# Kernel tuning notes

Measured on AMD Instinct MI355X. Metric: run time of the kernel, lower is better.

## Reference

```python
import jax, jax.numpy as jnp
import numpy as np
import math

B, T, D, H, P, NPASS = 2, 2048, 1024, 16, 256, 3


def setup_inputs() -> dict:
    key = jax.random.key(0)
    ks = jax.random.split(key, 8)
    x = jax.random.normal(ks[0], (B, T, D), jnp.float32)
    scale_gamma = 1.0 + 0.1 * jax.random.normal(ks[1], (D,), jnp.float32)
    scale_beta = 0.1 * jax.random.normal(ks[2], (D,), jnp.float32)
    qkv_w = 0.02 * jax.random.normal(ks[3], (3 * D, D), jnp.float32)
    o_w = 0.02 * jax.random.normal(ks[4], (D, D), jnp.float32)
    norm1_w = jnp.ones((D,), jnp.float32)
    norm2_w = jnp.ones((D,), jnp.float32)
    angles = 0.1 * jax.random.normal(ks[5], (NPASS, P), jnp.float32)
    gate = jnp.ones((NPASS, D), jnp.float32)
    bias = jnp.zeros((NPASS, D), jnp.float32)
    # seeded random permutations matching torch.manual_seed(42+p*1000); torch.randperm
    pis, pjs = [], []
    for p in range(NPASS):
        rng = np.random.RandomState(42 + p * 1000)
        perm = rng.permutation(D)
        pis.append(perm[:P])
        pjs.append(perm[P:2 * P])
    pi = jnp.asarray(np.stack(pis), jnp.int32)
    pj = jnp.asarray(np.stack(pjs), jnp.int32)
    return dict(x=x, scale_gamma=scale_gamma, scale_beta=scale_beta, qkv_w=qkv_w,
                o_w=o_w, norm1_w=norm1_w, norm2_w=norm2_w, angles=angles,
                gate=gate, bias=bias, pi=pi, pj=pj)


def _rmsnorm(x, w):
    eps = jnp.finfo(x.dtype).eps
    return x * jax.lax.rsqrt(jnp.mean(x * x, axis=-1, keepdims=True) + eps) * w


def reference(x, scale_gamma, scale_beta, qkv_w, o_w, norm1_w, norm2_w,
              angles, gate, bias, pi, pj):
    Bs, Ts, Ds = x.shape
    hd = Ds // H
    # --- attention branch ---
    h = _rmsnorm(x, norm1_w) * scale_gamma + scale_beta
    qkv = (h @ qkv_w.T).reshape(Bs, Ts, 3, H, hd)
    qkv = jnp.moveaxis(qkv, 2, 0)            # [3, B, T, H, hd]
    q, k, v = (jnp.swapaxes(qkv[i], 1, 2) for i in range(3))  # [B, H, T, hd]
    scores = jnp.einsum('bhqd,bhkd->bhqk', q, k) / math.sqrt(hd)
    causal = jnp.tril(jnp.ones((Ts, Ts), bool))
    scores = jnp.where(causal, scores, -jnp.inf)
    attn = jax.nn.softmax(scores, axis=-1)
    out = jnp.einsum('bhqk,bhkd->bhqd', attn, v)
    out = jnp.swapaxes(out, 1, 2).reshape(Bs, Ts, Ds)
    x = x + out @ o_w.T
    # --- rotation pseudo-FFN branch ---
    h = _rmsnorm(x, norm2_w) * scale_gamma + scale_beta
    r = h
    for p in range(NPASS):
        cos_a = jnp.cos(angles[p])
        sin_a = jnp.sin(angles[p])
        hi = r[..., pi[p]]
        hj = r[..., pj[p]]
        r = r.at[..., pi[p]].set(hi * cos_a - hj * sin_a)
        r = r.at[..., pj[p]].set(hi * sin_a + hj * cos_a)
        r = jax.nn.silu(r * gate[p] + bias[p])
    return x + r - h
```

## Files before the change

kernel.cpp:

```cpp
#include <hip/hip_runtime.h>
#include <hip/hip_bf16.h>

#define B_ 2
#define T_ 2048
#define D_ 1024
#define H_ 16
#define HD_ 64
#define NP_ 3
#define P_ 256

#define SCALE2 0.18033688011112042f

typedef short bf16x8 __attribute__((ext_vector_type(8)));
typedef float f32x4 __attribute__((ext_vector_type(4)));

__device__ __forceinline__ float bf2f(__hip_bfloat16 v) { return __bfloat162float(v); }
__device__ __forceinline__ __hip_bfloat16 f2bf(float v) { return __float2bfloat16(v); }

__device__ __forceinline__ unsigned pack2bf(float a, float b) {
    union { __hip_bfloat16 h; unsigned short u; } ua, ub;
    ua.h = f2bf(a); ub.h = f2bf(b);
    return (unsigned)ua.u | ((unsigned)ub.u << 16);
}

#define GLOAD_LDS16(gp, lp) \
    __builtin_amdgcn_global_load_lds( \
        (const __attribute__((address_space(1))) void*)(gp), \
        (__attribute__((address_space(3))) void*)(lp), 16, 0, 0)

__global__ __launch_bounds__(256) void detect_kernel(
    const unsigned short* __restrict__ xs, int* __restrict__ flag)
{
    __shared__ int cnt;
    if (threadIdx.x == 0) cnt = 0;
    __syncthreads();
    int bad = 0;
    for (int i = threadIdx.x; i < 16384; i += 256) {
        int e = (xs[i] >> 7) & 0xFF;
        if (e >= 0xB8) bad++;
    }
    if (bad) atomicAdd(&cnt, bad);
    __syncthreads();
    if (threadIdx.x == 0) *flag = (cnt >= 8) ? 1 : 0;
}

__global__ __launch_bounds__(256) void cvt16_2_kernel(
    const void* __restrict__ a, const void* __restrict__ bsrc,
    __hip_bfloat16* __restrict__ da, __hip_bfloat16* __restrict__ db,
    int na, int ntot, const int* __restrict__ flag)
{
    int i = blockIdx.x * 256 + threadIdx.x;
    if (i >= ntot) return;
    int f = *flag;
    if (i < na)
        da[i] = f ? f2bf(((const float*)a)[i]) : ((const __hip_bfloat16*)a)[i];
    else {
        int k = i - na;
        db[k] = f ? f2bf(((const float*)bsrc)[k]) : ((const __hip_bfloat16*)bsrc)[k];
    }
}

__global__ __launch_bounds__(256) void cvt_small_kernel(
    const void* __restrict__ g,  const void* __restrict__ b,
    const void* __restrict__ n1, const void* __restrict__ n2,
    const void* __restrict__ ang, const void* __restrict__ gt,
    const void* __restrict__ bi,
    float* __restrict__ dst, const int* __restrict__ flag)
{
    int i = blockIdx.x * 256 + threadIdx.x;
    if (i >= 11008) return;
    const void* src; int off;
    if      (i < 1024) { src = g;   off = i; }
    else if (i < 2048) { src = b;   off = i - 1024; }
    else if (i < 3072) { src = n1;  off = i - 2048; }
    else if (i < 4096) { src = n2;  off = i - 3072; }
    else if (i < 4864) { src = ang; off = i - 4096; }
    else if (i < 7936) { src = gt;  off = i - 4864; }
    else               { src = bi;  off = i - 7936; }
    dst[i] = (*flag) ? ((const float*)src)[off]
                     : bf2f(((const __hip_bfloat16*)src)[off]);
}

__global__ __launch_bounds__(256) void rmsnorm1_kernel(
    const void* __restrict__ xraw,
    const float* __restrict__ gamma,
    const float* __restrict__ beta,
    const float* __restrict__ w,
    const int* __restrict__ flag,
    __hip_bfloat16* __restrict__ out,
    float* __restrict__ xcopy)
{
    int row = blockIdx.x;
    int t = threadIdx.x;
    int f = *flag;
    float eps = f ? 1.1920929e-7f : 0.0078125f;
    float v[4];
    if (f) {
        const float4 xv = ((const float4*)((const float*)xraw + (size_t)row * D_))[t];
        v[0] = xv.x; v[1] = xv.y; v[2] = xv.z; v[3] = xv.w;
    } else {
        const __hip_bfloat16* xr = (const __hip_bfloat16*)xraw + (size_t)row * D_;
#pragma unroll
        for (int c = 0; c < 4; c++) v[c] = bf2f(xr[t * 4 + c]);
    }
    float ss = 0.f;
#pragma unroll
    for (int c = 0; c < 4; c++) ss += v[c] * v[c];
#pragma unroll
    for (int m = 32; m; m >>= 1) ss += __shfl_xor(ss, m, 64);
    __shared__ float red[4];
    int wv = t >> 6;
    if ((t & 63) == 0) red[wv] = ss;
    __syncthreads();
    float scale = rsqrtf((red[0] + red[1] + red[2] + red[3]) * (1.0f / D_) + eps);
#pragma unroll
    for (int c = 0; c < 4; c++) {
        int e = t * 4 + c;
        size_t idx = (size_t)row * D_ + e;
        xcopy[idx] = v[c];
        out[idx] = f2bf(v[c] * scale * w[e] * gamma[e] + beta[e]);
    }
}

__global__ __launch_bounds__(256) void gemm_bt_bf16_kernel(
    const __hip_bfloat16* __restrict__ A,
    const __hip_bfloat16* __restrict__ Bm,
    __hip_bfloat16* __restrict__ C,
    int M, int N, int K, int nscale, float qscale)
{
    __shared__ __attribute__((aligned(16))) __hip_bfloat16 As[128 * 32];
    __shared__ __attribute__((aligned(16))) __hip_bfloat16 Bs[128 * 32];
    int tid = threadIdx.x;
    int bm = blockIdx.y, bn = blockIdx.x;
    int lane = tid & 63, wv = tid >> 6;
    int wm = wv >> 1, wn = wv & 1;
    int q = lane >> 4, mr = lane & 15;

    f32x4 acc[4][4] = {};

    for (int k0 = 0; k0 < K; k0 += 32) {
#pragma unroll
        for (int s = 0; s < 2; s++) {
            int e = (s * 256 + tid) * 8;
            int r = e >> 5, c = e & 31;
            GLOAD_LDS16(&A[(size_t)(bm * 128 + r) * K + k0 + c], &As[e]);
            GLOAD_LDS16(&Bm[(size_t)(bn * 128 + r) * K + k0 + c], &Bs[e]);
        }
        __syncthreads();
        bf16x8 af[4], bfr[4];
#pragma unroll
        for (int i = 0; i < 4; i++)
            af[i] = *(const bf16x8*)(&As[(wm * 64 + i * 16 + mr) * 32 + q * 8]);
#pragma unroll
        for (int j = 0; j < 4; j++)
            bfr[j] = *(const bf16x8*)(&Bs[(wn * 64 + j * 16 + mr) * 32 + q * 8]);
#pragma unroll
        for (int i = 0; i < 4; i++)
#pragma unroll
            for (int j = 0; j < 4; j++)
                acc[i][j] = __builtin_amdgcn_mfma_f32_16x16x32_bf16(af[i], bfr[j], acc[i][j], 0, 0, 0);
        __syncthreads();
    }

#pragma unroll
    for (int i = 0; i < 4; i++)
#pragma unroll
        for (int r = 0; r < 4; r++) {
            int m = bm * 128 + wm * 64 + i * 16 + q * 4 + r;
#pragma unroll
            for (int j = 0; j < 4; j++) {
                int n = bn * 128 + wn * 64 + j * 16 + mr;
                float vv = acc[i][j][r];
                if (n < nscale) vv *= qscale;
                C[(size_t)m * N + n] = f2bf(vv);
            }
        }
}

__global__ __launch_bounds__(256) void gemm_bt_resid_kernel(
    const __hip_bfloat16* __restrict__ A,
    const __hip_bfloat16* __restrict__ Bm,
    const float* __restrict__ resid,
    float* __restrict__ C,
    int M, int N, int K)
{
    __shared__ __attribute__((aligned(16))) __hip_bfloat16 As[128 * 32];
    __shared__ __attribute__((aligned(16))) __hip_bfloat16 Bs[128 * 32];
    int tid = threadIdx.x;
    int bm = blockIdx.y, bn = blockIdx.x;
    int lane = tid & 63, wv = tid >> 6;
    int wm = wv >> 1, wn = wv & 1;
    int q = lane >> 4, mr = lane & 15;

    f32x4 acc[4][4] = {};

    for (int k0 = 0; k0 < K; k0 += 32) {
#pragma unroll
        for (int s = 0; s < 2; s++) {
            int e = (s * 256 + tid) * 8;
            int r = e >> 5, c = e & 31;
            GLOAD_LDS16(&A[(size_t)(bm * 128 + r) * K + k0 + c], &As[e]);
            GLOAD_LDS16(&Bm[(size_t)(bn * 128 + r) * K + k0 + c], &Bs[e]);
        }
        __syncthreads();
        bf16x8 af[4], bfr[4];
#pragma unroll
        for (int i = 0; i < 4; i++)
            af[i] = *(const bf16x8*)(&As[(wm * 64 + i * 16 + mr) * 32 + q * 8]);
#pragma unroll
        for (int j = 0; j < 4; j++)
            bfr[j] = *(const bf16x8*)(&Bs[(wn * 64 + j * 16 + mr) * 32 + q * 8]);
#pragma unroll
        for (int i = 0; i < 4; i++)
#pragma unroll
            for (int j = 0; j < 4; j++)
                acc[i][j] = __builtin_amdgcn_mfma_f32_16x16x32_bf16(af[i], bfr[j], acc[i][j], 0, 0, 0);
        __syncthreads();
    }

#pragma unroll
    for (int i = 0; i < 4; i++)
#pragma unroll
        for (int r = 0; r < 4; r++) {
            int m = bm * 128 + wm * 64 + i * 16 + q * 4 + r;
#pragma unroll
            for (int j = 0; j < 4; j++) {
                int n = bn * 128 + wn * 64 + j * 16 + mr;
                size_t idx = (size_t)m * N + n;
                C[idx] = resid[idx] + acc[i][j][r];
            }
        }
}

__global__ __launch_bounds__(256, 4) void attn_kernel(
    const __hip_bfloat16* __restrict__ qkv,
    __hip_bfloat16* __restrict__ attn_out)
{
    __shared__ __attribute__((aligned(16))) __hip_bfloat16 Ks[2][64 * 64];
    __shared__ __attribute__((aligned(16))) __hip_bfloat16 Vts[2][64 * 64];
    __shared__ __attribute__((aligned(16))) unsigned int Pd[4 * 512];

    int z = blockIdx.x;
    int qt0 = 31 - z, qt1 = z;
    int bh = blockIdx.y;
    int b = bh >> 4, h = bh & 15;
    int tid = threadIdx.x, lane = tid & 63, wv = tid >> 6;
    int q = lane >> 4, mr = lane & 15;
    int m8 = mr & 7;

    const size_t rs3 = 3 * D_;
    const __hip_bfloat16* qp = qkv + (size_t)(b * T_) * rs3 + h * HD_;
    const __hip_bfloat16* kp = qp + D_;
    const __hip_bfloat16* vp = qp + 2 * D_;

    int sr = tid >> 2;
    int sc = (tid & 3) * 16;
    int lc0 = sc >> 3;
    int swk = sr & 7;
    int kk_ = (tid & 31) * 2;
    int dd = (tid >> 5) * 8;
    int vlc = kk_ >> 3, voff = kk_ & 7;

    bf16x8 aq0, aq1, aqn0, aqn1;
    {
        const __hip_bfloat16* qrow = qp + (size_t)(qt0 * 64 + wv * 16 + mr) * rs3;
        aq0 = *(const bf16x8*)(qrow + q * 8);
        aq1 = *(const bf16x8*)(qrow + 32 + q * 8);
    }

    bf16x8 kr0 = *(const bf16x8*)(kp + (size_t)sr * rs3 + sc);
    bf16x8 kr1 = *(const bf16x8*)(kp + (size_t)sr * rs3 + sc + 8);
    bf16x8 vr0 = *(const bf16x8*)(vp + (size_t)kk_ * rs3 + dd);
    bf16x8 vr1 = *(const bf16x8*)(vp + (size_t)(kk_ + 1) * rs3 + dd);
    *(bf16x8*)(&Ks[0][sr * 64 + ((lc0 ^ swk) * 8)]) = kr0;
    *(bf16x8*)(&Ks[0][sr * 64 + (((lc0 + 1) ^ swk) * 8)]) = kr1;
    {
        unsigned int* vd = (unsigned int*)&Vts[0][0];
#pragma unroll
        for (int i = 0; i < 8; i++) {
            unsigned int wd = ((unsigned int)(unsigned short)vr0[i]) |
                              (((unsigned int)(unsigned short)vr1[i]) << 16);
            vd[((dd + i) * 64 + ((vlc ^ i) * 8 + voff)) >> 1] = wd;
        }
    }
    __syncthreads();

    float m_run = -INFINITY, l_run = 0.f;
    f32x4 o_acc[4] = {};
    unsigned int* Pw = &Pd[wv * 512];
    int qloc = wv * 16 + mr;

    for (int s = 0; s <= 32; s++) {
        int seg1 = (s > qt0);
        int kt = seg1 ? (s - qt0 - 1) : s;
        int qt = seg1 ? qt1 : qt0;
        int buf = s & 1;

        if (s < 32) {
            int ktn = (s + 1 > qt0) ? (s - qt0) : (s + 1);
            kr0 = *(const bf16x8*)(kp + (size_t)(ktn * 64 + sr) * rs3 + sc);
            kr1 = *(const bf16x8*)(kp + (size_t)(ktn * 64 + sr) * rs3 + sc + 8);
            vr0 = *(const bf16x8*)(vp + (size_t)(ktn * 64 + kk_) * rs3 + dd);
            vr1 = *(const bf16x8*)(vp + (size_t)(ktn * 64 + kk_ + 1) * rs3 + dd);
        }
        if (s == qt0) {
            const __hip_bfloat16* qrow = qp + (size_t)(qt1 * 64 + wv * 16 + mr) * rs3;
            aqn0 = *(const bf16x8*)(qrow + q * 8);
            aqn1 = *(const bf16x8*)(qrow + 32 + q * 8);
        }

        f32x4 sv[4] = {};
        {
            const __hip_bfloat16* Kb = &Ks[buf][0];
#pragma unroll
            for (int jn = 0; jn < 4; jn++)
                sv[jn] = __builtin_amdgcn_mfma_f32_16x16x32_bf16(
                    *(const bf16x8*)(&Kb[(jn * 16 + mr) * 64 + ((q ^ m8) * 8)]),
                    aq0, sv[jn], 0, 0, 0);
#pragma unroll
            for (int jn = 0; jn < 4; jn++)
                sv[jn] = __builtin_amdgcn_mfma_f32_16x16x32_bf16(
                    *(const bf16x8*)(&Kb[(jn * 16 + mr) * 64 + (((4 + q) ^ m8) * 8)]),
                    aq1, sv[jn], 0, 0, 0);
        }

        if (kt == qt) {
#pragma unroll
            for (int jn = 0; jn < 4; jn++)
#pragma unroll
                for (int r = 0; r < 4; r++)
                    if (jn * 16 + q * 4 + r > qloc) sv[jn][r] = -1e30f;
        }

        float mx = fmaxf(fmaxf(sv[0][0], sv[0][1]), fmaxf(sv[0][2], sv[0][3]));
#pragma unroll
        for (int jn = 1; jn < 4; jn++)
            mx = fmaxf(mx, fmaxf(fmaxf(sv[jn][0], sv[jn][1]), fmaxf(sv[jn][2], sv[jn][3])));
        mx = fmaxf(mx, __shfl_xor(mx, 16, 64));
        mx = fmaxf(mx, __shfl_xor(mx, 32, 64));
        float mn = fmaxf(m_run, mx);
        float alpha = exp2f(m_run - mn);
        m_run = mn;
        float psum = 0.f;
#pragma unroll
        for (int jn = 0; jn < 4; jn++)
#pragma unroll
            for (int r = 0; r < 4; r++) {
                float p = exp2f(sv[jn][r] - mn);
                sv[jn][r] = p;
                psum += p;
            }
        psum += __shfl_xor(psum, 16, 64);
        psum += __shfl_xor(psum, 32, 64);
        l_run = l_run * alpha + psum;
#pragma unroll
        for (int dt = 0; dt < 4; dt++)
#pragma unroll
            for (int r = 0; r < 4; r++)
                o_acc[dt][r] *= alpha;

#pragma unroll
        for (int jn = 0; jn < 4; jn++) {
            uint2 val;
            val.x = pack2bf(sv[jn][0], sv[jn][1]);
            val.y = pack2bf(sv[jn][2], sv[jn][3]);
            int dw4 = 2 * jn + (q >> 1);
            *(uint2*)(&Pw[mr * 32 + ((dw4 ^ m8) << 2) + 2 * (q & 1)]) = val;
        }

#pragma unroll
        for (int kk = 0; kk < 2; kk++) {
            bf16x8 bp = *(const bf16x8*)(&Pw[mr * 32 + (((4 * kk + q) ^ m8) << 2)]);
#pragma unroll
            for (int dt = 0; dt < 4; dt++) {
                bf16x8 bv = *(const bf16x8*)(&Vts[buf][(dt * 16 + mr) * 64 + (((kk * 4 + q) ^ m8) * 8)]);
                o_acc[dt] = __builtin_amdgcn_mfma_f32_16x16x32_bf16(bv, bp, o_acc[dt], 0, 0, 0);
            }
        }

        if (s < 32) {
            *(bf16x8*)(&Ks[buf ^ 1][sr * 64 + ((lc0 ^ swk) * 8)]) = kr0;
            *(bf16x8*)(&Ks[buf ^ 1][sr * 64 + (((lc0 + 1) ^ swk) * 8)]) = kr1;
            unsigned int* vd = (unsigned int*)&Vts[buf ^ 1][0];
#pragma unroll
            for (int i = 0; i < 8; i++) {
                unsigned int wd = ((unsigned int)(unsigned short)vr0[i]) |
                                  (((unsigned int)(unsigned short)vr1[i]) << 16);
                vd[((dd + i) * 64 + ((vlc ^ i) * 8 + voff)) >> 1] = wd;
            }
        }
        __syncthreads();

        if (s == qt0) {
            float inv = 1.0f / l_run;
            int trow = qt0 * 64 + wv * 16 + mr;
            __hip_bfloat16* op = attn_out + (size_t)(b * T_ + trow) * D_ + h * HD_;
#pragma unroll
            for (int dt = 0; dt < 4; dt++) {
                uint2 val;
                val.x = pack2bf(o_acc[dt][0] * inv, o_acc[dt][1] * inv);
                val.y = pack2bf(o_acc[dt][2] * inv, o_acc[dt][3] * inv);
                *(uint2*)(op + dt * 16 + q * 4) = val;
            }
            m_run = -INFINITY; l_run = 0.f;
#pragma unroll
            for (int dt = 0; dt < 4; dt++) o_acc[dt] = (f32x4){0.f, 0.f, 0.f, 0.f};
            aq0 = aqn0; aq1 = aqn1;
        }
    }

    {
        float inv = 1.0f / l_run;
        int trow = qt1 * 64 + wv * 16 + mr;
        __hip_bfloat16* op = attn_out + (size_t)(b * T_ + trow) * D_ + h * HD_;
#pragma unroll
        for (int dt = 0; dt < 4; dt++) {
            uint2 val;
            val.x = pack2bf(o_acc[dt][0] * inv, o_acc[dt][1] * inv);
            val.y = pack2bf(o_acc[dt][2] * inv, o_acc[dt][3] * inv);
            *(uint2*)(op + dt * 16 + q * 4) = val;
        }
    }
}

__global__ __launch_bounds__(256) void final_kernel(
    const float* __restrict__ xn,
    const float* __restrict__ gamma,
    const float* __restrict__ beta,
    const float* __restrict__ w2,
    const float* __restrict__ angles,
    const float* __restrict__ gate,
    const float* __restrict__ bias,
    const int* __restrict__ pi,
    const int* __restrict__ pj,
    const int* __restrict__ flag,
    void* __restrict__ outp)
{
    __shared__ float rbuf[D_];
    __shared__ float red[4];
    int row = blockIdx.x, t = threadIdx.x;
    int f = *flag;
    float eps = f ? 1.1920929e-7f : 0.0078125f;
    const float* xr = xn + (size_t)row * D_;
    float x4[4];
    float ss = 0.f;
#pragma unroll
    for (int c = 0; c < 4; c++) { x4[c] = xr[t * 4 + c]; ss += x4[c] * x4[c]; }
#pragma unroll
    for (int m = 32; m; m >>= 1) ss += __shfl_xor(ss, m, 64);
    int wv = t >> 6;
    if ((t & 63) == 0) red[wv] = ss;
    __syncthreads();
    float scale = rsqrtf((red[0] + red[1] + red[2] + red[3]) * (1.0f / D_) + eps);
    float hloc[4];
#pragma unroll
    for (int c = 0; c < 4; c++) {
        int e = t * 4 + c;
        float hv = x4[c] * scale * w2[e] * gamma[e] + beta[e];
        hloc[c] = hv;
        rbuf[e] = hv;
    }
    __syncthreads();
    for (int p = 0; p < NP_; p++) {
        float a = angles[p * P_ + t];
        float ca = __cosf(a), sa = __sinf(a);
        int ip = pi[p * P_ + t], jp = pj[p * P_ + t];
        float hi = rbuf[ip], hj = rbuf[jp];
        rbuf[ip] = hi * ca - hj * sa;
        rbuf[jp] = hi * sa + hj * ca;
        __syncthreads();
#pragma unroll
        for (int c = 0; c < 4; c++) {
            int e = t * 4 + c;
            float v = rbuf[e] * gate[p * D_ + e] + bias[p * D_ + e];
            rbuf[e] = v / (1.f + __expf(-v));
        }
        __syncthreads();
    }
#pragma unroll
    for (int c = 0; c < 4; c++) {
        int e = t * 4 + c;
        float ov = x4[c] + rbuf[e] - hloc[c];
        size_t idx = (size_t)row * D_ + e;
        if (f) ((float*)outp)[idx] = ov;
        else   ((__hip_bfloat16*)outp)[idx] = f2bf(ov);
    }
}

extern "C" void kernel_launch(void* const* d_in, const int* in_sizes, int n_in,
                              void* d_out, int out_size, void* d_ws, size_t ws_size,
                              hipStream_t stream)
{
    const void* x      = d_in[0];
    const void* gamma  = d_in[1];
    const void* beta   = d_in[2];
    const void* qkv_w  = d_in[3];
    const void* o_w    = d_in[4];
    const void* n1w    = d_in[5];
    const void* n2w    = d_in[6];
    const void* angles = d_in[7];
    const void* gate   = d_in[8];
    const void* bias   = d_in[9];
    const int* pi = (const int*)d_in[10];
    const int* pj = (const int*)d_in[11];

    const int M = B_ * T_;
    char* ws = (char*)d_ws;
    const size_t MB = 1u << 20;
    int*   flag   = (int*)ws;
    float* smalls = (float*)(ws + 4096);
    float* gf   = smalls;
    float* bf   = smalls + 1024;
    float* n1f  = smalls + 2048;
    float* n2f  = smalls + 3072;
    float* angf = smalls + 4096;
    float* gtf  = smalls + 4864;
    float* bif  = smalls + 7936;
    float*          xf32 = (float*)         (ws +  1 * MB);
    __hip_bfloat16* wbf  = (__hip_bfloat16*)(ws + 17 * MB);
    __hip_bfloat16* owbf = (__hip_bfloat16*)(ws + 23 * MB);
    __hip_bfloat16* h1   = (__hip_bfloat16*)(ws + 25 * MB);
    __hip_bfloat16* qkv  = (__hip_bfloat16*)(ws + 33 * MB);
    float*          xnew = (float*)         (ws + 33 * MB);

    detect_kernel<<<1, 256, 0, stream>>>((const unsigned short*)x, flag);

    cvt_small_kernel<<<43, 256, 0, stream>>>(gamma, beta, n1w, n2w, angles, gate, bias,
                                             smalls, flag);
    cvt16_2_kernel<<<(4 * D_ * D_ + 255) / 256, 256, 0, stream>>>(
        qkv_w, o_w, wbf, owbf, 3 * D_ * D_, 4 * D_ * D_, flag);

    rmsnorm1_kernel<<<M, 256, 0, stream>>>(x, gf, bf, n1f, flag, h1, xf32);

    gemm_bt_bf16_kernel<<<dim3(3 * D_ / 128, M / 128), 256, 0, stream>>>(
        h1, wbf, qkv, M, 3 * D_, D_, D_, SCALE2);

    attn_kernel<<<dim3(16, B_ * H_), 256, 0, stream>>>(qkv, h1);

    gemm_bt_resid_kernel<<<dim3(D_ / 128, M / 128), 256, 0, stream>>>(
        h1, owbf, xf32, xnew, M, D_, D_);

    final_kernel<<<M, 256, 0, stream>>>(xnew, gf, bf, n2f, angf, gtf, bif,
                                        pi, pj, flag, d_out);
}
```

Measured before the change: 257.8 us.

## Split attention into one block per query tile and drop fp32 residual copy

The attention kernel previously paired query tiles (31-z, z) in one block to balance causal work. It now launches 1024 blocks, each handling a single query tile, with an interleaved mapping that alternates short and long tiles so the scheduler can spread them. Separately, the rmsnorm kernel no longer writes an fp32 copy of x; the output-projection GEMM reads the original input (fp32 or bf16 per the flag) directly as the residual. This removes one full-activation write and read, but the per-block causal load is now unbalanced and relies on hardware scheduling to even it out.

```diff
diff --git a/kernel.cpp b/kernel.cpp
--- a/kernel.cpp
+++ b/kernel.cpp
@@ -87,8 +87,7 @@
     const float* __restrict__ beta,
     const float* __restrict__ w,
     const int* __restrict__ flag,
-    __hip_bfloat16* __restrict__ out,
-    float* __restrict__ xcopy)
+    __hip_bfloat16* __restrict__ out)
 {
     int row = blockIdx.x;
     int t = threadIdx.x;
@@ -117,7 +116,6 @@
     for (int c = 0; c < 4; c++) {
         int e = t * 4 + c;
         size_t idx = (size_t)row * D_ + e;
-        xcopy[idx] = v[c];
         out[idx] = f2bf(v[c] * scale * w[e] * gamma[e] + beta[e]);
     }
 }
@@ -180,7 +178,8 @@
 __global__ __launch_bounds__(256) void gemm_bt_resid_kernel(
     const __hip_bfloat16* __restrict__ A,
     const __hip_bfloat16* __restrict__ Bm,
-    const float* __restrict__ resid,
+    const void* __restrict__ xraw,
+    const int* __restrict__ flag,
     float* __restrict__ C,
     int M, int N, int K)
 {
@@ -191,6 +190,7 @@
     int lane = tid & 63, wv = tid >> 6;
     int wm = wv >> 1, wn = wv & 1;
     int q = lane >> 4, mr = lane & 15;
+    int f = *flag;
 
     f32x4 acc[4][4] = {};
 
@@ -227,7 +227,9 @@
             for (int j = 0; j < 4; j++) {
                 int n = bn * 128 + wn * 64 + j * 16 + mr;
                 size_t idx = (size_t)m * N + n;
-                C[idx] = resid[idx] + acc[i][j][r];
+                float rv = f ? ((const float*)xraw)[idx]
+                             : bf2f(((const __hip_bfloat16*)xraw)[idx]);
+                C[idx] = rv + acc[i][j][r];
             }
         }
 }
@@ -240,9 +242,11 @@
     __shared__ __attribute__((aligned(16))) __hip_bfloat16 Vts[2][64 * 64];
     __shared__ __attribute__((aligned(16))) unsigned int Pd[4 * 512];
 
-    int z = blockIdx.x;
-    int qt0 = 31 - z, qt1 = z;
-    int bh = blockIdx.y;
+    int id = blockIdx.x;
+    int half = (id ^ (id >> 8)) & 1;
+    int w4 = (id >> 1) & 15;
+    int qt = half ? 31 - w4 : w4;
+    int bh = (id >> 5) & 31;
     int b = bh >> 4, h = bh & 15;
     int tid = threadIdx.x, lane = tid & 63, wv = tid >> 6;
     int q = lane >> 4, mr = lane & 15;
@@ -261,9 +265,9 @@
     int dd = (tid >> 5) * 8;
     int vlc = kk_ >> 3, voff = kk_ & 7;
 
-    bf16x8 aq0, aq1, aqn0, aqn1;
+    bf16x8 aq0, aq1;
     {
-        const __hip_bfloat16* qrow = qp + (size_t)(qt0 * 64 + wv * 16 + mr) * rs3;
+        const __hip_bfloat16* qrow = qp + (size_t)(qt * 64 + wv * 16 + mr) * rs3;
         aq0 = *(const bf16x8*)(qrow + q * 8);
         aq1 = *(const bf16x8*)(qrow + 32 + q * 8);
     }
@@ -290,24 +294,16 @@
     unsigned int* Pw = &Pd[wv * 512];
     int qloc = wv * 16 + mr;
 
-    for (int s = 0; s <= 32; s++) {
-        int seg1 = (s > qt0);
-        int kt = seg1 ? (s - qt0 - 1) : s;
-        int qt = seg1 ? qt1 : qt0;
+    for (int s = 0; s <= qt; s++) {
         int buf = s & 1;
 
-        if (s < 32) {
-            int ktn = (s + 1 > qt0) ? (s - qt0) : (s + 1);
+        if (s < qt) {
+            int ktn = s + 1;
             kr0 = *(const bf16x8*)(kp + (size_t)(ktn * 64 + sr) * rs3 + sc);
             kr1 = *(const bf16x8*)(kp + (size_t)(ktn * 64 + sr) * rs3 + sc + 8);
             vr0 = *(const bf16x8*)(vp + (size_t)(ktn * 64 + kk_) * rs3 + dd);
             vr1 = *(const bf16x8*)(vp + (size_t)(ktn * 64 + kk_ + 1) * rs3 + dd);
         }
-        if (s == qt0) {
-            const __hip_bfloat16* qrow = qp + (size_t)(qt1 * 64 + wv * 16 + mr) * rs3;
-            aqn0 = *(const bf16x8*)(qrow + q * 8);
-            aqn1 = *(const bf16x8*)(qrow + 32 + q * 8);
-        }
 
         f32x4 sv[4] = {};
         {
@@ -324,7 +320,7 @@
                     aq1, sv[jn], 0, 0, 0);
         }
 
-        if (kt == qt) {
+        if (s == qt) {
 #pragma unroll
             for (int jn = 0; jn < 4; jn++)
 #pragma unroll
@@ -378,7 +374,7 @@
             }
         }
 
-        if (s < 32) {
+        if (s < qt) {
             *(bf16x8*)(&Ks[buf ^ 1][sr * 64 + ((lc0 ^ swk) * 8)]) = kr0;
             *(bf16x8*)(&Ks[buf ^ 1][sr * 64 + (((lc0 + 1) ^ swk) * 8)]) = kr1;
             unsigned int* vd = (unsigned int*)&Vts[buf ^ 1][0];
@@ -390,28 +386,11 @@
             }
         }
         __syncthreads();
-
-        if (s == qt0) {
-            float inv = 1.0f / l_run;
-            int trow = qt0 * 64 + wv * 16 + mr;
-            __hip_bfloat16* op = attn_out + (size_t)(b * T_ + trow) * D_ + h * HD_;
-#pragma unroll
-            for (int dt = 0; dt < 4; dt++) {
-                uint2 val;
-                val.x = pack2bf(o_acc[dt][0] * inv, o_acc[dt][1] * inv);
-                val.y = pack2bf(o_acc[dt][2] * inv, o_acc[dt][3] * inv);
-                *(uint2*)(op + dt * 16 + q * 4) = val;
-            }
-            m_run = -INFINITY; l_run = 0.f;
-#pragma unroll
-            for (int dt = 0; dt < 4; dt++) o_acc[dt] = (f32x4){0.f, 0.f, 0.f, 0.f};
-            aq0 = aqn0; aq1 = aqn1;
-        }
     }
 
     {
         float inv = 1.0f / l_run;
-        int trow = qt1 * 64 + wv * 16 + mr;
+        int trow = qt * 64 + wv * 16 + mr;
         __hip_bfloat16* op = attn_out + (size_t)(b * T_ + trow) * D_ + h * HD_;
 #pragma unroll
         for (int dt = 0; dt < 4; dt++) {
@@ -516,7 +495,6 @@
     float* angf = smalls + 4096;
     float* gtf  = smalls + 4864;
     float* bif  = smalls + 7936;
-    float*          xf32 = (float*)         (ws +  1 * MB);
     __hip_bfloat16* wbf  = (__hip_bfloat16*)(ws + 17 * MB);
     __hip_bfloat16* owbf = (__hip_bfloat16*)(ws + 23 * MB);
     __hip_bfloat16* h1   = (__hip_bfloat16*)(ws + 25 * MB);
@@ -530,15 +508,15 @@
     cvt16_2_kernel<<<(4 * D_ * D_ + 255) / 256, 256, 0, stream>>>(
         qkv_w, o_w, wbf, owbf, 3 * D_ * D_, 4 * D_ * D_, flag);
 
-    rmsnorm1_kernel<<<M, 256, 0, stream>>>(x, gf, bf, n1f, flag, h1, xf32);
+    rmsnorm1_kernel<<<M, 256, 0, stream>>>(x, gf, bf, n1f, flag, h1);
 
     gemm_bt_bf16_kernel<<<dim3(3 * D_ / 128, M / 128), 256, 0, stream>>>(
         h1, wbf, qkv, M, 3 * D_, D_, D_, SCALE2);
 
-    attn_kernel<<<dim3(16, B_ * H_), 256, 0, stream>>>(qkv, h1);
+    attn_kernel<<<dim3(1024), 256, 0, stream>>>(qkv, h1);
 
     gemm_bt_resid_kernel<<<dim3(D_ / 128, M / 128), 256, 0, stream>>>(
-        h1, owbf, xf32, xnew, M, D_, D_);
+        h1, owbf, x, flag, xnew, M, D_, D_);
 
     final_kernel<<<M, 256, 0, stream>>>(xnew, gf, bf, n2f, angf, gtf, bif,
                                         pi, pj, flag, d_out);
```

Result: no change. 255.6 us (-0.9%).
